# Kernel tuning notes

Hardware: AMD Instinct MI355X
Metric: run time of the kernel (lower is better)

## Reference

```python
import jax, jax.numpy as jnp
import numpy as np

N = 20
DM = 128
C_CLIP = 10.0
BATCH = 16384


def setup_inputs() -> dict:
    key = jax.random.key(0)
    ks = jax.random.split(key, 9)
    s = 1.0 / np.sqrt(DM)
    inp = {
        "x": jax.random.normal(ks[0], (BATCH, N, DM), dtype=jnp.float32),
        "Wg": jax.random.uniform(ks[1], (DM, DM), jnp.float32, -s, s),
        "bg": jax.random.uniform(ks[2], (DM,), jnp.float32, -s, s),
        "Wn": jax.random.uniform(ks[3], (DM, DM), jnp.float32, -s, s),
        "bn": jax.random.uniform(ks[4], (DM,), jnp.float32, -s, s),
        "Wk": jax.random.uniform(ks[5], (DM, DM), jnp.float32, -s, s),
        "bk": jax.random.uniform(ks[6], (DM,), jnp.float32, -s, s),
        "Wq": jax.random.uniform(ks[7], (DM, DM), jnp.float32, -s, s),
        "bq": jax.random.uniform(ks[8], (DM,), jnp.float32, -s, s),
    }
    return inp


def reference(x, Wg, bg, Wn, bn, Wk, bk, Wq, bq):
    B, n, dm = x.shape
    # graph embedding: max-pool over nodes
    x_graph = jnp.max(x, axis=1)                      # [B, dm]
    lp_graph = x_graph @ Wg.T + bg                    # [B, dm]
    lp_nodes = x @ Wn.T + bn                          # [B, n, dm]
    h = lp_nodes + lp_graph[:, None, :]               # [B, n, dm]
    K = h @ Wk.T + bk                                 # [B, n, dm]
    Q = h @ Wq.T + bq                                 # [B, n, dm]
    M = jnp.einsum("bnd,bmd->bnm", K, Q) / np.float32(np.sqrt(dm))
    M_hat = C_CLIP * jnp.tanh(M) - jnp.eye(n, dtype=M.dtype) * 1e20
    # flattened (global) softmax over all n*n entries
    p = jax.nn.softmax(M_hat.reshape(B, n * n), axis=1)
    return p.reshape(B, n, n)
```

## Files before the change

### kernel.cpp

```cpp
#include <hip/hip_runtime.h>
#include <hip/hip_bf16.h>
#include <math.h>

#define DM 128
#define NN 20
#define NB 16384
#define BPB 8

#define OFF_A      0
#define OFF_AT     16384
#define OFF_WA     32768
#define OFF_WAT    49152
#define OFF_AG     65536
#define OFF_BMAT   81920
#define OFF_S1T    98304
#define OFF_S2T    114688
#define OFF_C2T    131072
#define OFF_U0     147456
#define OFF_V0     147584
#define OFF_T0     147712
#define OFF_W1     147840
#define OFF_AT0    147968
#define OFF_A0     148096
#define OFF_B0     148224
#define OFF_C1     148352
#define OFF_C00    148480
#define OFF_CBASE  148481
#define OFF_FRAGB  149504
#define OFF_FRAGS  (149504 + 8192)

#define INVS 0.08838834764831845f
#define FW 132

typedef _Float16 h16;
typedef h16 half8 __attribute__((ext_vector_type(8)));
typedef h16 half4v __attribute__((ext_vector_type(4)));
typedef h16 half2v __attribute__((ext_vector_type(2)));
typedef float f32x4 __attribute__((ext_vector_type(4)));
typedef unsigned int uint4v __attribute__((ext_vector_type(4)));

#define MFMA16(a, b, c) __builtin_amdgcn_mfma_f32_16x16x32_f16((a), (b), (c), 0, 0, 0)

__device__ __forceinline__ int swz(int row, int col) {
    return (row * 128 + col) ^ ((row & 7) << 3);
}

__device__ __forceinline__ unsigned pkmax(unsigned a, unsigned b) {
    const half2v r = __builtin_elementwise_max(__builtin_bit_cast(half2v, a),
                                               __builtin_bit_cast(half2v, b));
    return __builtin_bit_cast(unsigned, r);
}

__device__ __forceinline__ int fb_idx(int k, int j) {
    return ((j >> 4) << 11) | ((k >> 5) << 9)
         | ((((k >> 3) & 3) * 16 + (j & 15)) << 3) | (k & 7);
}

__global__ void k_prep1(const float* __restrict__ Wk, const float* __restrict__ Wq,
                        const float* __restrict__ bk, const float* __restrict__ bq,
                        const float* __restrict__ bn, const float* __restrict__ bg,
                        float* __restrict__ ws) {
    const int bx = blockIdx.x, t = threadIdx.x;
    __shared__ float sbuf[128];
    if (bx < 128) {
        sbuf[t] = Wk[t * 128 + bx];
        __syncthreads();
        float a = 0.f;
        #pragma unroll 8
        for (int d = 0; d < 128; ++d) a += sbuf[d] * Wq[d * 128 + t];
        ws[OFF_A  + bx * 128 + t] = a;
        ws[OFF_AT + t * 128 + bx] = a;
    } else {
        float u = 0.f, v = 0.f;
        #pragma unroll 8
        for (int d = 0; d < 128; ++d) {
            u += Wk[d * 128 + t] * bq[d];
            v += Wq[d * 128 + t] * bk[d];
        }
        ws[OFF_U0 + t] = u;
        ws[OFF_V0 + t] = v;
        ws[OFF_T0 + t] = bn[t] + bg[t];
        sbuf[t] = bk[t] * bq[t];
        __syncthreads();
        for (int s = 64; s > 0; s >>= 1) { if (t < s) sbuf[t] += sbuf[t + s]; __syncthreads(); }
        if (t == 0) ws[OFF_C00] = sbuf[0];
    }
}

__global__ void k_prep2(const float* __restrict__ Wn, const float* __restrict__ Wg,
                        float* __restrict__ ws) {
    const int bx = blockIdx.x, t = threadIdx.x;
    __shared__ float s1[128], s2[128];
    if (bx < 128) {
        const int r = bx;
        s1[t] = Wn[t * 128 + r];
        s2[t] = ws[OFF_A + r * 128 + t];
        __syncthreads();
        float wa = 0.f, wat = 0.f, ag = 0.f;
        #pragma unroll 4
        for (int e = 0; e < 128; ++e) {
            wa  += s1[e] * ws[OFF_A  + e * 128 + t];
            wat += s1[e] * ws[OFF_AT + e * 128 + t];
            ag  += s2[e] * Wg[e * 128 + t];
        }
        ws[OFF_WA  + r * 128 + t] = wa;
        ws[OFF_WAT + r * 128 + t] = wat;
        ws[OFF_AG  + r * 128 + t] = ag;
    } else {
        const float t0t = ws[OFF_T0 + t], u0t = ws[OFF_U0 + t], v0t = ws[OFF_V0 + t];
        float w1 = 0.f, at0 = 0.f;
        #pragma unroll 8
        for (int e = 0; e < 128; ++e) {
            const float t0e = ws[OFF_T0 + e];
            w1  += (ws[OFF_A + t * 128 + e] + ws[OFF_AT + t * 128 + e]) * t0e;
            at0 +=  ws[OFF_A + t * 128 + e] * t0e;
        }
        w1 += u0t + v0t;
        ws[OFF_W1  + t] = w1;
        ws[OFF_AT0 + t] = at0;
        s1[t] = t0t * (at0 + u0t + v0t);
        __syncthreads();
        for (int s = 64; s > 0; s >>= 1) { if (t < s) s1[t] += s1[t + s]; __syncthreads(); }
        if (t == 0) ws[OFF_CBASE] = s1[0] + ws[OFF_C00];
    }
}

__global__ void k_prep3(const float* __restrict__ Wn, const float* __restrict__ Wg,
                        float* __restrict__ ws) {
    const int bx = blockIdx.x, t = threadIdx.x;
    __shared__ float wa[128], wat[128], wgc[128];
    h16* fB = (h16*)(ws + OFF_FRAGB);
    h16* fS = (h16*)(ws + OFF_FRAGS);
    if (bx < 128) {
        const int r = bx;
        wa[t]  = ws[OFF_WA  + r * 128 + t];
        wat[t] = ws[OFF_WAT + r * 128 + t];
        wgc[t] = Wg[t * 128 + r];
        __syncthreads();
        float bm = 0.f, s1v = 0.f, s2v = 0.f, c2v = 0.f;
        #pragma unroll 4
        for (int f = 0; f < 128; ++f) {
            bm  += wa[f]  * Wn[f * 128 + t];
            s1v += wa[f]  * Wg[f * 128 + t];
            s2v += wat[f] * Wg[f * 128 + t];
            c2v += wgc[f] * ws[OFF_AG + f * 128 + t];
        }
        fB[fb_idx(r, t)]       = (h16)bm;
        fS[fb_idx(t, r)]       = (h16)s1v;
        fS[fb_idx(t, r + 128)] = (h16)s2v;
        fS[fb_idx(t, r + 256)] = (h16)c2v;
    } else {
        float a0 = 0.f, b0 = 0.f, c1 = 0.f;
        #pragma unroll 8
        for (int f = 0; f < 128; ++f) {
            a0 += ws[OFF_WA  + t * 128 + f] * ws[OFF_T0 + f] + Wn[f * 128 + t] * ws[OFF_U0 + f];
            b0 += ws[OFF_WAT + t * 128 + f] * ws[OFF_T0 + f] + Wn[f * 128 + t] * ws[OFF_V0 + f];
            c1 += Wg[f * 128 + t] * ws[OFF_W1 + f];
        }
        ws[OFF_A0 + t] = a0;
        ws[OFF_B0 + t] = b0;
        ws[OFF_C1 + t] = c1;
    }
}

__global__ __launch_bounds__(512, 6) void k_fused(const float* __restrict__ x,
                                                  const float* __restrict__ ws,
                                                  float* __restrict__ out) {
    __shared__ __align__(16) h16 xgl[BPB * 128];
    __shared__ __align__(16) h16 avhL[BPB * 2 * 128];
    __shared__ __align__(16) h16 fFs[BPB * NN * FW];
    __shared__ float abL[BPB][40];
    __shared__ float cpart[BPB][BPB];
    __shared__ float cbs[BPB];

    const int t = threadIdx.x, l = t & 63, w = t >> 6;
    const int lc = l & 15, lg = l >> 4;
    const int b = blockIdx.x * BPB + w;
    const half8 h8z = {};

    const float* xb = x + (size_t)b * 2560;
    half8 xa0[4], xa1[4];
    #pragma unroll
    for (int ks = 0; ks < 4; ++ks) {
        const float4 v0 = *(const float4*)(xb + lc * 128 + 32 * ks + 8 * lg);
        const float4 v1 = *(const float4*)(xb + lc * 128 + 32 * ks + 8 * lg + 4);
        xa0[ks] = (half8){ (h16)v0.x, (h16)v0.y, (h16)v0.z, (h16)v0.w,
                           (h16)v1.x, (h16)v1.y, (h16)v1.z, (h16)v1.w };
    }
    #pragma unroll
    for (int ks = 0; ks < 4; ++ks) {
        half8 v = h8z;
        if (lc < 4) {
            const float4 v0 = *(const float4*)(xb + (16 + lc) * 128 + 32 * ks + 8 * lg);
            const float4 v1 = *(const float4*)(xb + (16 + lc) * 128 + 32 * ks + 8 * lg + 4);
            v = (half8){ (h16)v0.x, (h16)v0.y, (h16)v0.z, (h16)v0.w,
                         (h16)v1.x, (h16)v1.y, (h16)v1.z, (h16)v1.w };
        }
        xa1[ks] = v;
    }

    #pragma unroll
    for (int ks = 0; ks < 4; ++ks) {
        uint4v m0 = __builtin_bit_cast(uint4v, xa0[ks]);
        uint4v m1 = __builtin_bit_cast(uint4v, xa1[ks]);
        #pragma unroll
        for (int s = 1; s < 16; s <<= 1) {
            #pragma unroll
            for (int wd = 0; wd < 4; ++wd)
                m0[wd] = pkmax(m0[wd], (unsigned)__shfl_xor((int)m0[wd], s));
        }
        #pragma unroll
        for (int s = 1; s < 4; s <<= 1) {
            #pragma unroll
            for (int wd = 0; wd < 4; ++wd)
                m1[wd] = pkmax(m1[wd], (unsigned)__shfl_xor((int)m1[wd], s));
        }
        #pragma unroll
        for (int wd = 0; wd < 4; ++wd) {
            const unsigned m1b = (unsigned)__shfl((int)m1[wd], l & 51);
            m0[wd] = pkmax(m0[wd], m1b);
        }
        if (lc == 0)
            *(half8*)(xgl + swz(w, 32 * ks + 8 * lg)) = __builtin_bit_cast(half8, m0);
    }
    __syncthreads();

    {
        const half8* fS = (const half8*)(ws + OFF_FRAGS);
        f32x4 sacc[3];
        #pragma unroll
        for (int i = 0; i < 3; ++i) sacc[i] = (f32x4){0.f, 0.f, 0.f, 0.f};
        #pragma unroll
        for (int ks = 0; ks < 4; ++ks) {
            const half8 ag = *(const half8*)(xgl + swz(lc & 7, 32 * ks + 8 * lg));
            #pragma unroll
            for (int i = 0; i < 3; ++i) {
                const int ct = w + 8 * i;
                sacc[i] = MFMA16(ag, fS[(ct * 4 + ks) * 64 + l], sacc[i]);
            }
        }
        #pragma unroll
        for (int i = 0; i < 2; ++i) {
            const int ct = w + 8 * i;
            const int v = ct >> 3, c128 = 16 * (ct & 7) + lc;
            const float bias = (v == 0) ? ws[OFF_A0 + c128] : ws[OFF_B0 + c128];
            if (lg < 2) {
                #pragma unroll
                for (int r = 0; r < 4; ++r)
                    avhL[(4 * lg + r) * 256 + v * 128 + c128] = (h16)(sacc[i][r] + bias);
            }
        }
        {
            const int j = 16 * w + lc;
            const float c1j = ws[OFF_C1 + j];
            float p[4];
            #pragma unroll
            for (int r = 0; r < 4; ++r) {
                const float xgv = (float)xgl[swz((4 * lg + r) & 7, j)];
                p[r] = (sacc[2][r] + c1j) * xgv;
            }
            #pragma unroll
            for (int r = 0; r < 4; ++r) {
                float v = p[r];
                v += __shfl_xor(v, 1); v += __shfl_xor(v, 2);
                v += __shfl_xor(v, 4); v += __shfl_xor(v, 8);
                if (lc == 0 && lg < 2) cpart[4 * lg + r][w] = v;
            }
        }
    }
    __syncthreads();
    if (t < BPB) {
        float s = ws[OFF_CBASE];
        #pragma unroll
        for (int j = 0; j < BPB; ++j) s += cpart[t][j];
        cbs[t] = s;
    }
    __syncthreads();

    half8 s8[4];
    #pragma unroll
    for (int ks = 0; ks < 4; ++ks) {
        half8 v = h8z;
        if (lc < 2) v = *(const half8*)(avhL + w * 256 + lc * 128 + 32 * ks + 8 * lg);
        s8[ks] = v;
    }
    {
        f32x4 a0c = {0.f, 0.f, 0.f, 0.f}, a1c = {0.f, 0.f, 0.f, 0.f};
        #pragma unroll
        for (int ks = 0; ks < 4; ++ks) {
            a0c = MFMA16(xa0[ks], s8[ks], a0c);
            a1c = MFMA16(xa1[ks], s8[ks], a1c);
        }
        if (lc == 0) {
            #pragma unroll
            for (int r = 0; r < 4; ++r) abL[w][4 * lg + r] = a0c[r];
            if (lg == 0) {
                #pragma unroll
                for (int r = 0; r < 4; ++r) abL[w][16 + r] = a1c[r];
            }
        }
        if (lc == 1) {
            #pragma unroll
            for (int r = 0; r < 4; ++r) abL[w][20 + 4 * lg + r] = a0c[r];
            if (lg == 0) {
                #pragma unroll
                for (int r = 0; r < 4; ++r) abL[w][36 + r] = a1c[r];
            }
        }
    }

    h16* fFw = fFs + w * NN * FW;
    const half8* fB = (const half8*)(ws + OFF_FRAGB);

    #pragma unroll
    for (int ct = 0; ct < 8; ++ct) {
        f32x4 f0 = {0.f, 0.f, 0.f, 0.f}, f1 = {0.f, 0.f, 0.f, 0.f};
        #pragma unroll
        for (int ks = 0; ks < 4; ++ks) {
            const half8 bb = fB[(ct * 4 + ks) * 64 + l];
            f0 = MFMA16(xa0[ks], bb, f0);
            f1 = MFMA16(xa1[ks], bb, f1);
        }
        #pragma unroll
        for (int r = 0; r < 4; ++r) {
            fFw[(4 * lg + r) * FW + 16 * ct + lc] = (h16)f0[r];
            if (lg == 0) fFw[(16 + r) * FW + 16 * ct + lc] = (h16)f1[r];
        }
    }
    asm volatile("s_waitcnt lgkmcnt(0)" ::: "memory");

    f32x4 mAcc[2][2];
    #pragma unroll
    for (int nt = 0; nt < 2; ++nt)
        #pragma unroll
        for (int mt = 0; mt < 2; ++mt) mAcc[nt][mt] = (f32x4){0.f, 0.f, 0.f, 0.f};
    #pragma unroll
    for (int nt = 0; nt < 2; ++nt) {
        #pragma unroll
        for (int ks = 0; ks < 4; ++ks) {
            const int row = 16 * nt + lc;
            const half8 aF = *(const half8*)(fFw + (row < NN ? row : 0) * FW + 32 * ks + 8 * lg);
            mAcc[nt][0] = MFMA16(aF, xa0[ks], mAcc[nt][0]);
            mAcc[nt][1] = MFMA16(aF, xa1[ks], mAcc[nt][1]);
        }
    }

    const float cb = cbs[w];
    const float bm0 = abL[w][20 + lc];
    const float bm1 = (lc < 4) ? abL[w][36 + lc] : 0.f;
    float pv[2][2][4];
    float psum = 0.f;
    #pragma unroll
    for (int nt = 0; nt < 2; ++nt) {
        #pragma unroll
        for (int r = 0; r < 4; ++r) {
            const int n = 16 * nt + 4 * lg + r;
            const float an = (n < NN) ? abL[w][n] : 0.f;
            #pragma unroll
            for (int mt = 0; mt < 2; ++mt) {
                const int m = 16 * mt + lc;
                const bool valid = (n < NN) && (m < NN) && (n != m);
                const float Mv = (mAcc[nt][mt][r] + an + (mt ? bm1 : bm0) + cb) * INVS;
                const float E = __expf(2.f * Mv);
                const float e = valid ? __expf(-20.f / (E + 1.f)) : 0.f;
                pv[nt][mt][r] = e;
                psum += e;
            }
        }
    }
    #pragma unroll
    for (int off = 32; off > 0; off >>= 1) psum += __shfl_xor(psum, off);
    const float inv = 1.f / psum;

    float* ob = out + (size_t)b * 400;
    #pragma unroll
    for (int nt = 0; nt < 2; ++nt) {
        #pragma unroll
        for (int r = 0; r < 4; ++r) {
            const int n = 16 * nt + 4 * lg + r;
            if (n < NN) {
                ob[n * 20 + lc] = pv[nt][0][r] * inv;
                if (lc < 4) ob[n * 20 + 16 + lc] = pv[nt][1][r] * inv;
            }
        }
    }
}

extern "C" void kernel_launch(void* const* d_in, const int* in_sizes, int n_in,
                              void* d_out, int out_size, void* d_ws, size_t ws_size,
                              hipStream_t stream) {
    const float* x  = (const float*)d_in[0];
    const float* Wg = (const float*)d_in[1];
    const float* bg = (const float*)d_in[2];
    const float* Wn = (const float*)d_in[3];
    const float* bn = (const float*)d_in[4];
    const float* Wk = (const float*)d_in[5];
    const float* bk = (const float*)d_in[6];
    const float* Wq = (const float*)d_in[7];
    const float* bq = (const float*)d_in[8];
    float* out = (float*)d_out;
    float* ws  = (float*)d_ws;

    k_prep1<<<129, 128, 0, stream>>>(Wk, Wq, bk, bq, bn, bg, ws);
    k_prep2<<<129, 128, 0, stream>>>(Wn, Wg, ws);
    k_prep3<<<129, 128, 0, stream>>>(Wn, Wg, ws);
    k_fused<<<NB / BPB, 512, 0, stream>>>(x, ws, out);
}
```

Measured before the change: 115.2 us.

## Keep intermediate GEMM result in registers via lane shuffles instead of LDS

```diff
diff --git a/kernel.cpp b/kernel.cpp
--- a/kernel.cpp
+++ b/kernel.cpp
@@ -30,7 +30,6 @@
 #define OFF_FRAGS  (149504 + 8192)
 
 #define INVS 0.08838834764831845f
-#define FW 132
 
 typedef _Float16 h16;
 typedef h16 half8 __attribute__((ext_vector_type(8)));
@@ -49,6 +48,11 @@
     const half2v r = __builtin_elementwise_max(__builtin_bit_cast(half2v, a),
                                                __builtin_bit_cast(half2v, b));
     return __builtin_bit_cast(unsigned, r);
+}
+
+__device__ __forceinline__ unsigned pk2(float a, float b) {
+    const half2v p = { (h16)a, (h16)b };
+    return __builtin_bit_cast(unsigned, p);
 }
 
 __device__ __forceinline__ int fb_idx(int k, int j) {
@@ -168,7 +172,6 @@
                                                   float* __restrict__ out) {
     __shared__ __align__(16) h16 xgl[BPB * 128];
     __shared__ __align__(16) h16 avhL[BPB * 2 * 128];
-    __shared__ __align__(16) h16 fFs[BPB * NN * FW];
     __shared__ float abL[BPB][40];
     __shared__ float cpart[BPB][BPB];
     __shared__ float cbs[BPB];
@@ -309,61 +312,75 @@
         }
     }
 
-    h16* fFw = fFs + w * NN * FW;
     const half8* fB = (const half8*)(ws + OFF_FRAGB);
-
-    #pragma unroll
-    for (int ct = 0; ct < 8; ++ct) {
-        f32x4 f0 = {0.f, 0.f, 0.f, 0.f}, f1 = {0.f, 0.f, 0.f, 0.f};
-        #pragma unroll
-        for (int ks = 0; ks < 4; ++ks) {
-            const half8 bb = fB[(ct * 4 + ks) * 64 + l];
-            f0 = MFMA16(xa0[ks], bb, f0);
-            f1 = MFMA16(xa1[ks], bb, f1);
-        }
-        #pragma unroll
-        for (int r = 0; r < 4; ++r) {
-            fFw[(4 * lg + r) * FW + 16 * ct + lc] = (h16)f0[r];
-            if (lg == 0) fFw[(16 + r) * FW + 16 * ct + lc] = (h16)f1[r];
+    f32x4 macc[2][2];
+    #pragma unroll
+    for (int mt = 0; mt < 2; ++mt)
+        #pragma unroll
+        for (int ctn = 0; ctn < 2; ++ctn) macc[mt][ctn] = (f32x4){0.f, 0.f, 0.f, 0.f};
+    const bool hs = (l < 32);
+    const int s1 = lc + ((l >> 4) & 1) * 32;
+    const int s2 = s1 + 16;
+    #pragma unroll
+    for (int km = 0; km < 4; ++km) {
+        unsigned P[2][2][2];
+        #pragma unroll
+        for (int rp = 0; rp < 2; ++rp) {
+            const int rt = 2 * km + rp;
+            f32x4 f0 = {0.f, 0.f, 0.f, 0.f}, f1 = {0.f, 0.f, 0.f, 0.f};
+            #pragma unroll
+            for (int ks = 0; ks < 4; ++ks) {
+                const half8 a = fB[(rt * 4 + ks) * 64 + l];
+                f0 = MFMA16(a, xa0[ks], f0);
+                f1 = MFMA16(a, xa1[ks], f1);
+            }
+            P[rp][0][0] = pk2(f0[0], f0[1]); P[rp][0][1] = pk2(f0[2], f0[3]);
+            P[rp][1][0] = pk2(f1[0], f1[1]); P[rp][1][1] = pk2(f1[2], f1[3]);
+        }
+        #pragma unroll
+        for (int ctn = 0; ctn < 2; ++ctn) {
+            const unsigned A0 = (unsigned)__shfl((int)P[0][ctn][0], s1);
+            const unsigned B0 = (unsigned)__shfl((int)P[1][ctn][0], s1);
+            const unsigned A1 = (unsigned)__shfl((int)P[0][ctn][1], s1);
+            const unsigned B1 = (unsigned)__shfl((int)P[1][ctn][1], s1);
+            const unsigned A2 = (unsigned)__shfl((int)P[0][ctn][0], s2);
+            const unsigned B2 = (unsigned)__shfl((int)P[1][ctn][0], s2);
+            const unsigned A3 = (unsigned)__shfl((int)P[0][ctn][1], s2);
+            const unsigned B3 = (unsigned)__shfl((int)P[1][ctn][1], s2);
+            const uint4v uu = { hs ? A0 : B0, hs ? A1 : B1,
+                                hs ? A2 : B2, hs ? A3 : B3 };
+            const half8 bX = __builtin_bit_cast(half8, uu);
+            macc[0][ctn] = MFMA16(xa0[km], bX, macc[0][ctn]);
+            macc[1][ctn] = MFMA16(xa1[km], bX, macc[1][ctn]);
         }
     }
     asm volatile("s_waitcnt lgkmcnt(0)" ::: "memory");
 
-    f32x4 mAcc[2][2];
-    #pragma unroll
-    for (int nt = 0; nt < 2; ++nt)
-        #pragma unroll
-        for (int mt = 0; mt < 2; ++mt) mAcc[nt][mt] = (f32x4){0.f, 0.f, 0.f, 0.f};
-    #pragma unroll
-    for (int nt = 0; nt < 2; ++nt) {
-        #pragma unroll
-        for (int ks = 0; ks < 4; ++ks) {
-            const int row = 16 * nt + lc;
-            const half8 aF = *(const half8*)(fFw + (row < NN ? row : 0) * FW + 32 * ks + 8 * lg);
-            mAcc[nt][0] = MFMA16(aF, xa0[ks], mAcc[nt][0]);
-            mAcc[nt][1] = MFMA16(aF, xa1[ks], mAcc[nt][1]);
-        }
-    }
-
     const float cb = cbs[w];
-    const float bm0 = abL[w][20 + lc];
-    const float bm1 = (lc < 4) ? abL[w][36 + lc] : 0.f;
+    const float an0 = abL[w][lc];
+    const float an1 = (lc < 4) ? abL[w][16 + lc] : 0.f;
+    float bmv0[4], bmv1[4];
+    #pragma unroll
+    for (int r = 0; r < 4; ++r) {
+        bmv0[r] = abL[w][20 + 4 * lg + r];
+        bmv1[r] = (lg == 0) ? abL[w][36 + r] : 0.f;
+    }
     float pv[2][2][4];
     float psum = 0.f;
     #pragma unroll
-    for (int nt = 0; nt < 2; ++nt) {
-        #pragma unroll
-        for (int r = 0; r < 4; ++r) {
-            const int n = 16 * nt + 4 * lg + r;
-            const float an = (n < NN) ? abL[w][n] : 0.f;
-            #pragma unroll
-            for (int mt = 0; mt < 2; ++mt) {
-                const int m = 16 * mt + lc;
-                const bool valid = (n < NN) && (m < NN) && (n != m);
-                const float Mv = (mAcc[nt][mt][r] + an + (mt ? bm1 : bm0) + cb) * INVS;
+    for (int mt = 0; mt < 2; ++mt) {
+        #pragma unroll
+        for (int ctn = 0; ctn < 2; ++ctn) {
+            #pragma unroll
+            for (int r = 0; r < 4; ++r) {
+                const int n = 16 * ctn + lc;
+                const int m = 16 * mt + 4 * lg + r;
+                const bool valid = (ctn == 0 || lc < 4) && (mt == 0 || lg == 0) && (n != m);
+                const float Mv = (macc[mt][ctn][r] + (ctn ? an1 : an0)
+                                  + (mt ? bmv1[r] : bmv0[r]) + cb) * INVS;
                 const float E = __expf(2.f * Mv);
                 const float e = valid ? __expf(-20.f / (E + 1.f)) : 0.f;
-                pv[nt][mt][r] = e;
+                pv[mt][ctn][r] = e;
                 psum += e;
             }
         }
@@ -374,13 +391,16 @@
 
     float* ob = out + (size_t)b * 400;
     #pragma unroll
-    for (int nt = 0; nt < 2; ++nt) {
-        #pragma unroll
-        for (int r = 0; r < 4; ++r) {
-            const int n = 16 * nt + 4 * lg + r;
-            if (n < NN) {
-                ob[n * 20 + lc] = pv[nt][0][r] * inv;
-                if (lc < 4) ob[n * 20 + 16 + lc] = pv[nt][1][r] * inv;
+    for (int ctn = 0; ctn < 2; ++ctn) {
+        if (ctn == 0 || lc < 4) {
+            const int n = 16 * ctn + lc;
+            #pragma unroll
+            for (int mt = 0; mt < 2; ++mt) {
+                if (mt == 0 || lg == 0) {
+                    const f32x4 o = { pv[mt][ctn][0] * inv, pv[mt][ctn][1] * inv,
+                                      pv[mt][ctn][2] * inv, pv[mt][ctn][3] * inv };
+                    *(f32x4*)(ob + n * 20 + 16 * mt + 4 * lg) = o;
+                }
             }
         }
     }
```

After: 120.7 us. 1.05x slower.
